# Performance work log

Measured on AMD Instinct MI355X. Metric: run time of the kernel, lower is better.

The kernel has to match this reference:

```python
import jax, jax.numpy as jnp
import numpy as np

NQ = 5          # qubits
DIM = 2 ** NQ   # 32 amplitudes
NL = 4          # StronglyEntanglingLayers depth


def _rot_matrix(phi, theta, omega):
    """PennyLane Rot(phi,theta,omega) = RZ(omega) @ RY(theta) @ RZ(phi)."""
    c = jnp.cos(theta / 2)
    s = jnp.sin(theta / 2)
    ep = jnp.exp(-0.5j * (phi + omega).astype(jnp.complex64))
    em = jnp.exp(-0.5j * (phi - omega).astype(jnp.complex64))
    return jnp.array([[0, 0], [0, 0]], jnp.complex64).at[0, 0].set(ep * c).at[0, 1].set(-jnp.conj(em) * s).at[1, 0].set(em * s).at[1, 1].set(jnp.conj(ep) * c)


def _apply_1q(state, U, w):
    # state: (B, 2,2,2,2,2); apply 2x2 U on qubit axis w
    state = jnp.moveaxis(state, w + 1, -1)
    state = state @ U.T
    return jnp.moveaxis(state, -1, w + 1)


def _apply_cnot(state, c, t):
    # flip target axis on the control=1 slice
    s0 = jax.lax.index_in_dim(state, 0, axis=c + 1, keepdims=True)
    s1 = jax.lax.index_in_dim(state, 1, axis=c + 1, keepdims=True)
    s1 = jnp.flip(s1, axis=t + 1)
    return jnp.concatenate([s0, s1], axis=c + 1)


def setup_inputs() -> dict:
    key = jax.random.key(0)
    k1, k2 = jax.random.split(key)
    inputs = jax.random.normal(k1, (524288, 30), dtype=jnp.float32)
    weights = jax.random.normal(k2, (NL, NQ, 3), dtype=jnp.float32)
    return {"inputs": inputs, "weights": weights}


def reference(inputs, weights):
    B = inputs.shape[0]
    # AmplitudeEmbedding: pad with zeros to 32 amplitudes, normalize per sample
    padded = jnp.pad(inputs, ((0, 0), (0, DIM - inputs.shape[1])))
    norm = jnp.linalg.norm(padded, axis=1, keepdims=True)
    state = (padded / norm).astype(jnp.complex64)
    state = state.reshape((B,) + (2,) * NQ)

    # StronglyEntanglingLayers
    for l in range(NL):
        for w in range(NQ):
            U = _rot_matrix(weights[l, w, 0], weights[l, w, 1], weights[l, w, 2])
            state = _apply_1q(state, U, w)
        r = (l % (NQ - 1)) + 1  # default imprimitive range pattern
        for w in range(NQ):
            state = _apply_cnot(state, w, (w + r) % NQ)

    # expval(PauliZ(i)) for each wire
    probs = jnp.abs(state) ** 2  # (B,2,2,2,2,2)
    evs = []
    for w in range(NQ):
        axes = tuple(a for a in range(1, NQ + 1) if a != w + 1)
        p = probs.sum(axis=axes)  # (B,2)
        evs.append(p[:, 0] - p[:, 1])
    return jnp.stack(evs, axis=1)  # (B, NQ)
```

## Files before the change

### kernel.cpp

```cpp
#include <hip/hip_runtime.h>

#define NQ 5
#define DIM 32
#define NL 4
#define NFEAT 30
#define NGATES (NL * NQ)

typedef float f32x4 __attribute__((ext_vector_type(4)));
typedef float f32x2 __attribute__((ext_vector_type(2)));
typedef short bf16x8 __attribute__((ext_vector_type(8)));

static __device__ __forceinline__ unsigned short f2bf(float f) {
    unsigned u = __float_as_uint(f);
    u += 0x7FFFu + ((u >> 16) & 1u);
    return (unsigned short)(u >> 16);
}

__global__ __launch_bounds__(1024) void build_unitary(const float* __restrict__ W,
                                                      unsigned short* __restrict__ Ubf) {
    __shared__ float g[NGATES][8];

    const int t = threadIdx.x;
    if (t < NGATES) {
        const float phi = W[t * 3 + 0];
        const float th  = W[t * 3 + 1];
        const float om  = W[t * 3 + 2];
        const float c = cosf(0.5f * th), s = sinf(0.5f * th);
        const float a  = 0.5f * (phi + om);
        const float bb = 0.5f * (phi - om);
        const float epr = cosf(a),  epi = -sinf(a);
        const float emr = cosf(bb), emi = -sinf(bb);
        g[t][0] = epr * c;   g[t][1] = epi * c;
        g[t][2] = -emr * s;  g[t][3] = emi * s;
        g[t][4] = emr * s;   g[t][5] = emi * s;
        g[t][6] = epr * c;   g[t][7] = -epi * c;
    }
    __syncthreads();

    const int j = t >> 5;
    const int z = t & 31;

    float ar = (z == j) ? 1.0f : 0.0f;
    float ai = 0.0f;

#pragma unroll
    for (int l = 0; l < NL; ++l) {
#pragma unroll
        for (int w = 0; w < NQ; ++w) {
            const int gi = l * NQ + w;
            const int shift = 4 - w;
            const int msk = 1 << shift;
            const int bit = (z >> shift) & 1;
            const float pr = __shfl_xor(ar, msk, 32);
            const float pi = __shfl_xor(ai, msk, 32);
            const float csr = bit ? g[gi][6] : g[gi][0];
            const float csi = bit ? g[gi][7] : g[gi][1];
            const float cpr = bit ? g[gi][4] : g[gi][2];
            const float cpi = bit ? g[gi][5] : g[gi][3];
            const float nar = csr * ar - csi * ai + cpr * pr - cpi * pi;
            const float nai = csr * ai + csi * ar + cpr * pi + cpi * pr;
            ar = nar; ai = nai;
        }
        const int r = (l % (NQ - 1)) + 1;
#pragma unroll
        for (int cq = 0; cq < NQ; ++cq) {
            const int tq = (cq + r) % NQ;
            const int cs = 4 - cq, ts = 4 - tq;
            const int tmask = 1 << ts;
            const float pr = __shfl_xor(ar, tmask, 32);
            const float pi = __shfl_xor(ai, tmask, 32);
            const int ctrl = (z >> cs) & 1;
            ar = ctrl ? pr : ar;
            ai = ctrl ? pi : ai;
        }
    }

    Ubf[(2 * z + 0) * 32 + j] = f2bf(ar);
    Ubf[(2 * z + 1) * 32 + j] = f2bf(ai);
}

__global__ __launch_bounds__(256) void qforward(const float* __restrict__ X,
                                                const unsigned short* __restrict__ Ubf,
                                                float* __restrict__ out, int B) {
    __shared__ float outbuf[256 * NQ];
    const int tid  = threadIdx.x;
    const int b0   = blockIdx.x * 256;
    const int lane = tid & 63;
    const int g    = lane >> 4;
    const int r    = lane & 15;
    const int wv   = tid >> 6;

    bf16x8 afrag[4];
#pragma unroll
    for (int t = 0; t < 4; ++t)
        afrag[t] = *reinterpret_cast<const bf16x8*>(Ubf + (16 * t + r) * 32 + g * 8);

    f32x2 raw[4][4];
#pragma unroll
    for (int st = 0; st < 4; ++st) {
        int srow = b0 + wv * 64 + st * 16 + r;
        srow = min(srow, B - 1);
        const float* rowp = X + (long)srow * NFEAT + g * 8;
        raw[st][0] = *reinterpret_cast<const f32x2*>(rowp + 0);
        raw[st][1] = *reinterpret_cast<const f32x2*>(rowp + 2);
        raw[st][2] = *reinterpret_cast<const f32x2*>(rowp + 4);
        raw[st][3] = (g == 3) ? (f32x2){0.f, 0.f}
                              : *reinterpret_cast<const f32x2*>(rowp + 6);
    }

    const float sg2 = (g & 2) ? -1.f : 1.f;
    const float sg3 = (g & 1) ? -1.f : 1.f;

#pragma unroll
    for (int st = 0; st < 4; ++st) {
        bf16x8 bfrag;
#pragma unroll
        for (int q = 0; q < 4; ++q) {
            bfrag[2 * q + 0] = (short)f2bf(raw[st][q].x);
            bfrag[2 * q + 1] = (short)f2bf(raw[st][q].y);
        }

        f32x4 d[4];
#pragma unroll
        for (int t = 0; t < 4; ++t)
            d[t] = __builtin_amdgcn_mfma_f32_16x16x32_bf16(
                afrag[t], bfrag, (f32x4){0.f, 0.f, 0.f, 0.f}, 0, 0, 0);

        float ev0 = 0.f, ev1 = 0.f, ev2 = 0.f, ev3 = 0.f, ev4 = 0.f, nrm = 0.f;
#pragma unroll
        for (int t = 0; t < 4; ++t) {
            const float p0 = d[t].x * d[t].x + d[t].y * d[t].y;
            const float p1 = d[t].z * d[t].z + d[t].w * d[t].w;
            const float pt = p0 + p1;
            nrm += pt;
            ev0 += (t & 2) ? -pt : pt;
            ev1 += (t & 1) ? -pt : pt;
            ev2 = fmaf(sg2, pt, ev2);
            ev3 = fmaf(sg3, pt, ev3);
            ev4 += p0 - p1;
        }
        ev0 += __shfl_xor(ev0, 16, 64); ev0 += __shfl_xor(ev0, 32, 64);
        ev1 += __shfl_xor(ev1, 16, 64); ev1 += __shfl_xor(ev1, 32, 64);
        ev2 += __shfl_xor(ev2, 16, 64); ev2 += __shfl_xor(ev2, 32, 64);
        ev3 += __shfl_xor(ev3, 16, 64); ev3 += __shfl_xor(ev3, 32, 64);
        ev4 += __shfl_xor(ev4, 16, 64); ev4 += __shfl_xor(ev4, 32, 64);
        nrm += __shfl_xor(nrm, 16, 64); nrm += __shfl_xor(nrm, 32, 64);

        if (g == 0) {
            const float inv = 1.0f / nrm;
            const int s = wv * 64 + st * 16 + r;
            outbuf[s * NQ + 0] = ev0 * inv;
            outbuf[s * NQ + 1] = ev1 * inv;
            outbuf[s * NQ + 2] = ev2 * inv;
            outbuf[s * NQ + 3] = ev3 * inv;
            outbuf[s * NQ + 4] = ev4 * inv;
        }
    }

    __syncthreads();
    const int nrows = min(256, B - b0);
    const int ototal = nrows * NQ;
    for (int k = tid; k < ototal; k += 256)
        out[(long)b0 * NQ + k] = outbuf[k];
}

extern "C" void kernel_launch(void* const* d_in, const int* in_sizes, int n_in,
                              void* d_out, int out_size, void* d_ws, size_t ws_size,
                              hipStream_t stream) {
    const float* X = (const float*)d_in[0];
    const float* W = (const float*)d_in[1];
    float* out = (float*)d_out;
    const int B = in_sizes[0] / NFEAT;

    unsigned short* Ubf = (unsigned short*)d_ws;

    build_unitary<<<1, 1024, 0, stream>>>(W, Ubf);

    const int nblocks = (B + 255) / 256;
    qforward<<<nblocks, 256, 0, stream>>>(X, Ubf, out, B);
}
```

Baseline: 25.40 us.

## Stage input tile through LDS with coalesced 16-byte loads and packed bf16 conversion

Each block now loads its contiguous 256×30 float input tile into shared memory with coalesced 16-byte vector loads. Fragments are then read from LDS, which replaces the strided 8-byte per-row global loads. Float-to-bf16 conversion switches to the hardware packed convert instruction instead of manual rounding. The LDS buffer is reused for output staging, and a launch-bounds occupancy hint is added. In exchange, the extra barriers and the roughly 30 KB of LDS per block may limit occupancy.

```diff
diff --git a/kernel.cpp b/kernel.cpp
--- a/kernel.cpp
+++ b/kernel.cpp
@@ -14,6 +14,12 @@
     unsigned u = __float_as_uint(f);
     u += 0x7FFFu + ((u >> 16) & 1u);
     return (unsigned short)(u >> 16);
+}
+
+static __device__ __forceinline__ unsigned cvt_pk_bf16(float a, float b) {
+    unsigned d;
+    asm("v_cvt_pk_bf16_f32 %0, %1, %2" : "=v"(d) : "v"(a), "v"(b));
+    return d;
 }
 
 __global__ __launch_bounds__(1024) void build_unitary(const float* __restrict__ W,
@@ -79,10 +85,10 @@
     Ubf[(2 * z + 1) * 32 + j] = f2bf(ai);
 }
 
-__global__ __launch_bounds__(256) void qforward(const float* __restrict__ X,
-                                                const unsigned short* __restrict__ Ubf,
-                                                float* __restrict__ out, int B) {
-    __shared__ float outbuf[256 * NQ];
+__global__ __launch_bounds__(256, 5) void qforward(const float* __restrict__ X,
+                                                   const unsigned short* __restrict__ Ubf,
+                                                   float* __restrict__ out, int B) {
+    __shared__ __align__(16) float xs[256 * NFEAT];
     const int tid  = threadIdx.x;
     const int b0   = blockIdx.x * 256;
     const int lane = tid & 63;
@@ -95,30 +101,38 @@
     for (int t = 0; t < 4; ++t)
         afrag[t] = *reinterpret_cast<const bf16x8*>(Ubf + (16 * t + r) * 32 + g * 8);
 
-    f32x2 raw[4][4];
-#pragma unroll
-    for (int st = 0; st < 4; ++st) {
-        int srow = b0 + wv * 64 + st * 16 + r;
-        srow = min(srow, B - 1);
-        const float* rowp = X + (long)srow * NFEAT + g * 8;
-        raw[st][0] = *reinterpret_cast<const f32x2*>(rowp + 0);
-        raw[st][1] = *reinterpret_cast<const f32x2*>(rowp + 2);
-        raw[st][2] = *reinterpret_cast<const f32x2*>(rowp + 4);
-        raw[st][3] = (g == 3) ? (f32x2){0.f, 0.f}
-                              : *reinterpret_cast<const f32x2*>(rowp + 6);
-    }
+    const f32x4* __restrict__ X4 = reinterpret_cast<const f32x4*>(X) + (long)blockIdx.x * 1920;
+    const int tot4 = min(1920, ((B - b0) * NFEAT + 3) >> 2);
+#pragma unroll
+    for (int it = 0; it < 8; ++it) {
+        const int idx = tid + it * 256;
+        if (idx < tot4)
+            *reinterpret_cast<f32x4*>(&xs[idx * 4]) = X4[idx];
+    }
+    __syncthreads();
 
     const float sg2 = (g & 2) ? -1.f : 1.f;
     const float sg3 = (g & 1) ? -1.f : 1.f;
 
+    float evA[4][6];
+
 #pragma unroll
     for (int st = 0; st < 4; ++st) {
+        const int srow = wv * 64 + st * 16 + r;
+        const float* rowp = &xs[srow * NFEAT + g * 8];
+
+        f32x2 v0 = *reinterpret_cast<const f32x2*>(rowp + 0);
+        f32x2 v1 = *reinterpret_cast<const f32x2*>(rowp + 2);
+        f32x2 v2 = *reinterpret_cast<const f32x2*>(rowp + 4);
+        f32x2 v3 = (g == 3) ? (f32x2){0.f, 0.f}
+                            : *reinterpret_cast<const f32x2*>(rowp + 6);
+
         bf16x8 bfrag;
-#pragma unroll
-        for (int q = 0; q < 4; ++q) {
-            bfrag[2 * q + 0] = (short)f2bf(raw[st][q].x);
-            bfrag[2 * q + 1] = (short)f2bf(raw[st][q].y);
-        }
+        unsigned* bw = reinterpret_cast<unsigned*>(&bfrag);
+        bw[0] = cvt_pk_bf16(v0.x, v0.y);
+        bw[1] = cvt_pk_bf16(v1.x, v1.y);
+        bw[2] = cvt_pk_bf16(v2.x, v2.y);
+        bw[3] = cvt_pk_bf16(v3.x, v3.y);
 
         f32x4 d[4];
 #pragma unroll
@@ -146,18 +160,27 @@
         ev4 += __shfl_xor(ev4, 16, 64); ev4 += __shfl_xor(ev4, 32, 64);
         nrm += __shfl_xor(nrm, 16, 64); nrm += __shfl_xor(nrm, 32, 64);
 
-        if (g == 0) {
-            const float inv = 1.0f / nrm;
+        evA[st][0] = ev0; evA[st][1] = ev1; evA[st][2] = ev2;
+        evA[st][3] = ev3; evA[st][4] = ev4;
+        evA[st][5] = 1.0f / nrm;
+    }
+
+    __syncthreads();
+    float* outbuf = xs;
+    if (g == 0) {
+#pragma unroll
+        for (int st = 0; st < 4; ++st) {
             const int s = wv * 64 + st * 16 + r;
-            outbuf[s * NQ + 0] = ev0 * inv;
-            outbuf[s * NQ + 1] = ev1 * inv;
-            outbuf[s * NQ + 2] = ev2 * inv;
-            outbuf[s * NQ + 3] = ev3 * inv;
-            outbuf[s * NQ + 4] = ev4 * inv;
-        }
-    }
-
-    __syncthreads();
+            const float inv = evA[st][5];
+            outbuf[s * NQ + 0] = evA[st][0] * inv;
+            outbuf[s * NQ + 1] = evA[st][1] * inv;
+            outbuf[s * NQ + 2] = evA[st][2] * inv;
+            outbuf[s * NQ + 3] = evA[st][3] * inv;
+            outbuf[s * NQ + 4] = evA[st][4] * inv;
+        }
+    }
+    __syncthreads();
+
     const int nrows = min(256, B - b0);
     const int ototal = nrows * NQ;
     for (int k = tid; k < ototal; k += 256)
```

New measurement: 29.45 us. 16.0% more time.
